# Kernel tuning notes

Measured on AMD Instinct MI355X. Metric: run time of the kernel, lower is better.

The kernel has to match this reference:

```python
import jax, jax.numpy as jnp
import numpy as np

N_HEADS = 8
N_HIDDEN = 16  # out_features 128 / 8 heads
NEG_SLOPE = 0.2


def setup_inputs() -> dict:
    key = jax.random.key(0)
    k_h, k_adj, k_wl, k_wr, k_a = jax.random.split(key, 5)
    N, IN_F = 1024, 200
    OUT_F = N_HEADS * N_HIDDEN
    h = jax.random.normal(k_h, (1, N, IN_F), dtype=jnp.float32)
    adj = jax.random.randint(k_adj, (1, N, N), 0, 2, dtype=jnp.int32)
    # guarantee self-loops so no softmax row is fully masked
    adj = adj.at[0, jnp.arange(N), jnp.arange(N)].set(1)
    s_in = 1.0 / np.sqrt(IN_F)
    s_hid = 1.0 / np.sqrt(N_HIDDEN)
    W_l = jax.random.uniform(k_wl, (IN_F, OUT_F), jnp.float32, -s_in, s_in)
    W_r = jax.random.uniform(k_wr, (IN_F, OUT_F), jnp.float32, -s_in, s_in)
    attn_w = jax.random.uniform(k_a, (N_HIDDEN,), jnp.float32, -s_hid, s_hid)
    return {"h": h, "adj_mat": adj, "W_l": W_l, "W_r": W_r, "attn_w": attn_w}


def reference(h, adj_mat, W_l, W_r, attn_w):
    # h: [1, N, in_f]  (batch must be 1, as in the torch module)
    N = h.shape[1]
    x = h[0]                                   # [N, in_f]
    g_l = (x @ W_l).reshape(N, N_HEADS, N_HIDDEN)   # [N, H, F]
    g_r = (x @ W_r).reshape(N, N_HEADS, N_HIDDEN)   # [N, H, F]
    # g_sum[i, j, h, f] = g_r[i] + g_l[j]  (matches repeat/repeat_interleave)
    g_sum = g_r[:, None, :, :] + g_l[None, :, :, :]       # [N, N, H, F]
    e = jnp.einsum('ijhf,f->ijh',
                   jax.nn.leaky_relu(g_sum, NEG_SLOPE), attn_w)  # [N, N, H]
    mask = (adj_mat[0] != 0)[:, :, None]                  # [N, N, 1]
    e = jnp.where(mask, e, -jnp.inf)
    a = jax.nn.softmax(e, axis=1)                         # softmax over j
    # dropout is identity at inference
    out = jnp.einsum('ijh,jhf->ihf', a, g_r)              # [N, H, F]
    return out.reshape(1, N, N_HEADS * N_HIDDEN)
```

## Files before the change

### kernel.cpp

```cpp
#include <hip/hip_runtime.h>

#define NH 8
#define NF 16
#define NNODE 1024
#define INF_F 200
#define OUTF 128
#define IT 16
#define JS 8
#define JCH 64
#define NCH (NNODE / JS / JCH)
#define ESTR (JCH + 2)
#define NEG_INF (-__builtin_huge_valf())

__global__ __launch_bounds__(256) void proj_kernel(
        const float* __restrict__ x,
        const float* __restrict__ Wl,
        const float* __restrict__ Wr,
        float* __restrict__ gl,
        float* __restrict__ gr) {
    __shared__ float xs[8 * INF_F];
    const float* __restrict__ W = blockIdx.y ? Wr : Wl;
    float* __restrict__ g = blockIdx.y ? gr : gl;
    const int i0 = blockIdx.x * 8;
    const int tid = threadIdx.x;

    {
        const float4* src = (const float4*)(x + i0 * INF_F);
        float4* dst = (float4*)xs;
        for (int t = tid; t < (8 * INF_F) / 4; t += 256) dst[t] = src[t];
    }
    __syncthreads();

    const int c = tid & 127;
    const int r0 = (tid >> 7) * 4;
    float acc[4] = {0.f, 0.f, 0.f, 0.f};
#pragma unroll 4
    for (int k = 0; k < INF_F; ++k) {
        const float w = W[k * OUTF + c];
#pragma unroll
        for (int r = 0; r < 4; ++r)
            acc[r] = fmaf(xs[(r0 + r) * INF_F + k], w, acc[r]);
    }
#pragma unroll
    for (int r = 0; r < 4; ++r)
        g[(i0 + r0 + r) * OUTF + c] = acc[r];
}

__global__ __launch_bounds__(512) void gat_partial(
        const float* __restrict__ gl,
        const float* __restrict__ gr,
        const int* __restrict__ adj,
        const float* __restrict__ attn_w,
        float* __restrict__ outp,
        float* __restrict__ pm,
        float* __restrict__ ps) {
    __shared__ float gri[IT][OUTF];
    __shared__ float e_lds[NH][IT][ESTR];

    const int bid = blockIdx.x;
    const int itile = bid >> 3;
    const int js = bid & 7;
    const int i0 = itile * IT;
    const int tid = threadIdx.x;
    const int h = tid >> 6;
    const int lane = tid & 63;

    *(float4*)((float*)gri + tid * 4) = *(const float4*)(gr + i0 * OUTF + tid * 4);
    __syncthreads();

    float w[NF];
#pragma unroll
    for (int f = 0; f < NF; ++f) w[f] = attn_w[f];

    const int iq = lane >> 2;
    const int fq = lane & 3;
    float4 acc = {0.f, 0.f, 0.f, 0.f};
    float s_reg = 0.f;
    float m_reg = NEG_INF;

    for (int c = 0; c < NCH; ++c) {
        const int jbase = js * (NNODE / JS) + c * JCH;

        {
            const int row = jbase + lane;
            float glr[NF];
            {
                const float4* gp = (const float4*)(gl + row * OUTF + h * NF);
                float4 g0 = gp[0], g1 = gp[1], g2 = gp[2], g3 = gp[3];
                glr[0]=g0.x; glr[1]=g0.y; glr[2]=g0.z; glr[3]=g0.w;
                glr[4]=g1.x; glr[5]=g1.y; glr[6]=g1.z; glr[7]=g1.w;
                glr[8]=g2.x; glr[9]=g2.y; glr[10]=g2.z; glr[11]=g2.w;
                glr[12]=g3.x; glr[13]=g3.y; glr[14]=g3.z; glr[15]=g3.w;
            }
#pragma unroll
            for (int i = 0; i < IT; ++i) {
                const float4* ap = (const float4*)(&gri[i][h * NF]);
                float4 a0 = ap[0], a1 = ap[1], a2 = ap[2], a3 = ap[3];
                float ga[NF] = {a0.x,a0.y,a0.z,a0.w, a1.x,a1.y,a1.z,a1.w,
                                a2.x,a2.y,a2.z,a2.w, a3.x,a3.y,a3.z,a3.w};
                float ei = 0.f;
#pragma unroll
                for (int f = 0; f < NF; ++f) {
                    float v = ga[f] + glr[f];
                    v = fmaxf(v, 0.2f * v);
                    ei = fmaf(v, w[f], ei);
                }
                const int msk = adj[(i0 + i) * NNODE + row];
                e_lds[h][i][lane] = msk ? ei : NEG_INF;
            }
        }
        __syncthreads();

        {
            const float* er = &e_lds[h][iq][0];
            float m0 = NEG_INF, m1 = NEG_INF, m2 = NEG_INF, m3 = NEG_INF;
#pragma unroll
            for (int j = 0; j < JCH; j += 4) {
                m0 = fmaxf(m0, er[j]);
                m1 = fmaxf(m1, er[j + 1]);
                m2 = fmaxf(m2, er[j + 2]);
                m3 = fmaxf(m3, er[j + 3]);
            }
            const float m_c = fmaxf(fmaxf(m0, m1), fmaxf(m2, m3));
            const float m_new = fmaxf(m_reg, m_c);
            float mb, scale;
            if (m_new == NEG_INF) { mb = 0.f; scale = 0.f; }
            else { mb = m_new; scale = __expf(m_reg - m_new); }
            acc.x *= scale; acc.y *= scale; acc.z *= scale; acc.w *= scale;
            s_reg *= scale;
#pragma unroll 8
            for (int j = 0; j < JCH; ++j) {
                const float p = __expf(er[j] - mb);
                const float4 g = *(const float4*)(gr + (jbase + j) * OUTF + h * NF + fq * 4);
                acc.x = fmaf(p, g.x, acc.x);
                acc.y = fmaf(p, g.y, acc.y);
                acc.z = fmaf(p, g.z, acc.z);
                acc.w = fmaf(p, g.w, acc.w);
                s_reg += p;
            }
            m_reg = m_new;
        }
        __syncthreads();
    }

    {
        const int gi = i0 + iq;
        *(float4*)(outp + js * NNODE * OUTF + gi * OUTF + h * NF + fq * 4) = acc;
        if (fq == 0) {
            pm[js * NNODE * NH + gi * NH + h] = m_reg;
            ps[js * NNODE * NH + gi * NH + h] = s_reg;
        }
    }
}

__global__ __launch_bounds__(256) void gat_reduce(
        const float* __restrict__ outp,
        const float* __restrict__ pm,
        const float* __restrict__ ps,
        float* __restrict__ out) {
    const int t = blockIdx.x * 256 + threadIdx.x;
    const int i = t >> 7;
    const int c = t & 127;
    const int h = c >> 4;
    float m[JS];
    float M = NEG_INF;
#pragma unroll
    for (int s = 0; s < JS; ++s) {
        m[s] = pm[s * NNODE * NH + i * NH + h];
        M = fmaxf(M, m[s]);
    }
    float num = 0.f, den = 0.f;
#pragma unroll
    for (int s = 0; s < JS; ++s) {
        const float sc = (m[s] == NEG_INF) ? 0.f : __expf(m[s] - M);
        num = fmaf(outp[s * NNODE * OUTF + i * OUTF + c], sc, num);
        den = fmaf(ps[s * NNODE * NH + i * NH + h], sc, den);
    }
    out[t] = num / den;
}

extern "C" void kernel_launch(void* const* d_in, const int* in_sizes, int n_in,
                              void* d_out, int out_size, void* d_ws, size_t ws_size,
                              hipStream_t stream) {
    const float* h   = (const float*)d_in[0];
    const int*   adj = (const int*)d_in[1];
    const float* Wl  = (const float*)d_in[2];
    const float* Wr  = (const float*)d_in[3];
    const float* aw  = (const float*)d_in[4];
    float* out = (float*)d_out;

    float* gl   = (float*)d_ws;
    float* gr   = gl + NNODE * OUTF;
    float* outp = gr + NNODE * OUTF;
    float* pm   = outp + JS * NNODE * OUTF;
    float* ps   = pm + JS * NNODE * NH;

    proj_kernel<<<dim3(128, 2), 256, 0, stream>>>(h, Wl, Wr, gl, gr);
    gat_partial<<<dim3(64 * JS), 512, 0, stream>>>(gl, gr, adj, aw, outp, pm, ps);
    gat_reduce<<<dim3(NNODE * OUTF / 256), 256, 0, stream>>>(outp, pm, ps, out);
}
```

Measured before the change: 109.0 us.

## Split attention into single-chunk blocks with wave-level softmax and split-j accumulation

Each block now covers 8 query rows and one 64-column j chunk, with 16 j-splits, instead of looping over two chunks with 16 rows. The max and sum of the softmax are computed with wave shuffles while scores are produced, so LDS holds probabilities, not raw scores, and the online-rescale loop is gone. The aggregation splits j across lane pairs and merges them with a shuffle, and launch bounds request higher occupancy. The cost is a grid of 2048 blocks and twice as many partials for the reduce kernel to read and combine.

New measurement: 131.6 us. +20.7%, slower.

```diff
diff --git a/kernel.cpp b/kernel.cpp
--- a/kernel.cpp
+++ b/kernel.cpp
@@ -5,10 +5,9 @@
 #define NNODE 1024
 #define INF_F 200
 #define OUTF 128
-#define IT 16
-#define JS 8
+#define IT 8
+#define JS 16
 #define JCH 64
-#define NCH (NNODE / JS / JCH)
 #define ESTR (JCH + 2)
 #define NEG_INF (-__builtin_huge_valf())
 
@@ -46,7 +45,7 @@
         g[(i0 + r0 + r) * OUTF + c] = acc[r];
 }
 
-__global__ __launch_bounds__(512) void gat_partial(
+__global__ __launch_bounds__(512, 8) void gat_partial(
         const float* __restrict__ gl,
         const float* __restrict__ gr,
         const int* __restrict__ adj,
@@ -55,101 +54,88 @@
         float* __restrict__ pm,
         float* __restrict__ ps) {
     __shared__ float gri[IT][OUTF];
-    __shared__ float e_lds[NH][IT][ESTR];
+    __shared__ float p_lds[NH][IT][ESTR];
 
     const int bid = blockIdx.x;
-    const int itile = bid >> 3;
-    const int js = bid & 7;
+    const int itile = bid >> 4;
+    const int js = bid & 15;
     const int i0 = itile * IT;
+    const int jbase = js * JCH;
     const int tid = threadIdx.x;
     const int h = tid >> 6;
     const int lane = tid & 63;
 
-    *(float4*)((float*)gri + tid * 4) = *(const float4*)(gr + i0 * OUTF + tid * 4);
+    *(float2*)((float*)gri + tid * 2) = *(const float2*)(gr + i0 * OUTF + tid * 2);
     __syncthreads();
 
     float w[NF];
 #pragma unroll
     for (int f = 0; f < NF; ++f) w[f] = attn_w[f];
 
-    const int iq = lane >> 2;
-    const int fq = lane & 3;
-    float4 acc = {0.f, 0.f, 0.f, 0.f};
-    float s_reg = 0.f;
-    float m_reg = NEG_INF;
-
-    for (int c = 0; c < NCH; ++c) {
-        const int jbase = js * (NNODE / JS) + c * JCH;
-
+    {
+        const int row = jbase + lane;
+        float glr[NF];
         {
-            const int row = jbase + lane;
-            float glr[NF];
-            {
-                const float4* gp = (const float4*)(gl + row * OUTF + h * NF);
-                float4 g0 = gp[0], g1 = gp[1], g2 = gp[2], g3 = gp[3];
-                glr[0]=g0.x; glr[1]=g0.y; glr[2]=g0.z; glr[3]=g0.w;
-                glr[4]=g1.x; glr[5]=g1.y; glr[6]=g1.z; glr[7]=g1.w;
-                glr[8]=g2.x; glr[9]=g2.y; glr[10]=g2.z; glr[11]=g2.w;
-                glr[12]=g3.x; glr[13]=g3.y; glr[14]=g3.z; glr[15]=g3.w;
+            const float4* gp = (const float4*)(gl + row * OUTF + h * NF);
+            float4 g0 = gp[0], g1 = gp[1], g2 = gp[2], g3 = gp[3];
+            glr[0]=g0.x; glr[1]=g0.y; glr[2]=g0.z; glr[3]=g0.w;
+            glr[4]=g1.x; glr[5]=g1.y; glr[6]=g1.z; glr[7]=g1.w;
+            glr[8]=g2.x; glr[9]=g2.y; glr[10]=g2.z; glr[11]=g2.w;
+            glr[12]=g3.x; glr[13]=g3.y; glr[14]=g3.z; glr[15]=g3.w;
+        }
+#pragma unroll
+        for (int i = 0; i < IT; ++i) {
+            const float4* ap = (const float4*)(&gri[i][h * NF]);
+            const float4 a0 = ap[0], a1 = ap[1], a2 = ap[2], a3 = ap[3];
+            const float ga[NF] = {a0.x,a0.y,a0.z,a0.w, a1.x,a1.y,a1.z,a1.w,
+                                  a2.x,a2.y,a2.z,a2.w, a3.x,a3.y,a3.z,a3.w};
+            float e = 0.f;
+#pragma unroll
+            for (int f = 0; f < NF; ++f) {
+                float v = ga[f] + glr[f];
+                v = fmaxf(v, 0.2f * v);
+                e = fmaf(v, w[f], e);
             }
+            const int msk = adj[(i0 + i) * NNODE + row];
+            e = msk ? e : NEG_INF;
+            float m = e;
 #pragma unroll
-            for (int i = 0; i < IT; ++i) {
-                const float4* ap = (const float4*)(&gri[i][h * NF]);
-                float4 a0 = ap[0], a1 = ap[1], a2 = ap[2], a3 = ap[3];
-                float ga[NF] = {a0.x,a0.y,a0.z,a0.w, a1.x,a1.y,a1.z,a1.w,
-                                a2.x,a2.y,a2.z,a2.w, a3.x,a3.y,a3.z,a3.w};
-                float ei = 0.f;
+            for (int d = 1; d < 64; d <<= 1) m = fmaxf(m, __shfl_xor(m, d, 64));
+            const float p = (e == NEG_INF) ? 0.f : __expf(e - m);
+            float s = p;
 #pragma unroll
-                for (int f = 0; f < NF; ++f) {
-                    float v = ga[f] + glr[f];
-                    v = fmaxf(v, 0.2f * v);
-                    ei = fmaf(v, w[f], ei);
-                }
-                const int msk = adj[(i0 + i) * NNODE + row];
-                e_lds[h][i][lane] = msk ? ei : NEG_INF;
+            for (int d = 1; d < 64; d <<= 1) s += __shfl_xor(s, d, 64);
+            p_lds[h][i][lane] = p;
+            if (lane == i) {
+                pm[js * NNODE * NH + (i0 + i) * NH + h] = m;
+                ps[js * NNODE * NH + (i0 + i) * NH + h] = s;
             }
         }
-        __syncthreads();
-
-        {
-            const float* er = &e_lds[h][iq][0];
-            float m0 = NEG_INF, m1 = NEG_INF, m2 = NEG_INF, m3 = NEG_INF;
-#pragma unroll
-            for (int j = 0; j < JCH; j += 4) {
-                m0 = fmaxf(m0, er[j]);
-                m1 = fmaxf(m1, er[j + 1]);
-                m2 = fmaxf(m2, er[j + 2]);
-                m3 = fmaxf(m3, er[j + 3]);
-            }
-            const float m_c = fmaxf(fmaxf(m0, m1), fmaxf(m2, m3));
-            const float m_new = fmaxf(m_reg, m_c);
-            float mb, scale;
-            if (m_new == NEG_INF) { mb = 0.f; scale = 0.f; }
-            else { mb = m_new; scale = __expf(m_reg - m_new); }
-            acc.x *= scale; acc.y *= scale; acc.z *= scale; acc.w *= scale;
-            s_reg *= scale;
-#pragma unroll 8
-            for (int j = 0; j < JCH; ++j) {
-                const float p = __expf(er[j] - mb);
-                const float4 g = *(const float4*)(gr + (jbase + j) * OUTF + h * NF + fq * 4);
-                acc.x = fmaf(p, g.x, acc.x);
-                acc.y = fmaf(p, g.y, acc.y);
-                acc.z = fmaf(p, g.z, acc.z);
-                acc.w = fmaf(p, g.w, acc.w);
-                s_reg += p;
-            }
-            m_reg = m_new;
-        }
-        __syncthreads();
     }
+    __syncthreads();
 
     {
-        const int gi = i0 + iq;
-        *(float4*)(outp + js * NNODE * OUTF + gi * OUTF + h * NF + fq * 4) = acc;
-        if (fq == 0) {
-            pm[js * NNODE * NH + gi * NH + h] = m_reg;
-            ps[js * NNODE * NH + gi * NH + h] = s_reg;
+        const int iq = lane >> 3;
+        const int fq = (lane >> 1) & 3;
+        const int jh = lane & 1;
+        const float* pr = &p_lds[h][iq][jh * 32];
+        const float* grb = gr + (jbase + jh * 32) * OUTF + h * NF + fq * 4;
+        float4 acc = {0.f, 0.f, 0.f, 0.f};
+#pragma unroll 8
+        for (int t = 0; t < 32; ++t) {
+            const float p = pr[t];
+            const float4 g = *(const float4*)(grb + t * OUTF);
+            acc.x = fmaf(p, g.x, acc.x);
+            acc.y = fmaf(p, g.y, acc.y);
+            acc.z = fmaf(p, g.z, acc.z);
+            acc.w = fmaf(p, g.w, acc.w);
         }
+        acc.x += __shfl_xor(acc.x, 1, 64);
+        acc.y += __shfl_xor(acc.y, 1, 64);
+        acc.z += __shfl_xor(acc.z, 1, 64);
+        acc.w += __shfl_xor(acc.w, 1, 64);
+        if (jh == 0)
+            *(float4*)(outp + js * NNODE * OUTF + (i0 + iq) * OUTF + h * NF + fq * 4) = acc;
     }
 }
 
@@ -196,6 +182,6 @@
     float* ps   = pm + JS * NNODE * NH;
 
     proj_kernel<<<dim3(128, 2), 256, 0, stream>>>(h, Wl, Wr, gl, gr);
-    gat_partial<<<dim3(64 * JS), 512, 0, stream>>>(gl, gr, adj, aw, outp, pm, ps);
+    gat_partial<<<dim3((NNODE / IT) * JS), 512, 0, stream>>>(gl, gr, adj, aw, outp, pm, ps);
     gat_reduce<<<dim3(NNODE * OUTF / 256), 256, 0, stream>>>(outp, pm, ps, out);
 }
```
